# Performance work log

Measured on AMD Instinct MI355X. Metric: run time of the kernel, lower is better.

## Reference

```python
import jax, jax.numpy as jnp
import numpy as np

B, E, N, D, L = 16, 1024, 2048, 256, 3


def setup_inputs() -> dict:
    key = jax.random.key(0)
    ks = jax.random.split(key, 8)
    return {
        "evidences_mat": jax.random.normal(ks[0], (B, E, D), jnp.float32),
        "entities_mat": jax.random.normal(ks[1], (B, N, D), jnp.float32),
        "ev_to_ent": jax.random.bernoulli(ks[2], 0.05, (B, E, N)).astype(jnp.float32),
        "ent_to_ev": jax.random.bernoulli(ks[3], 0.05, (B, N, E)).astype(jnp.float32),
        "w_weight": jax.random.normal(ks[4], (L, D, D), jnp.float32) * 0.05,
        "w_bias": jax.random.normal(ks[5], (L, D), jnp.float32) * 0.05,
        "watt_weight": jax.random.normal(ks[6], (L, D, D), jnp.float32) * 0.05,
        "watt_bias": jax.random.normal(ks[7], (L, D), jnp.float32) * 0.05,
    }


def reference(evidences_mat, entities_mat, ev_to_ent, ent_to_ev,
              w_weight, w_bias, watt_weight, watt_bias):
    ev, ent = evidences_mat, entities_mat
    for i in range(L):
        # attention projections (torch Linear: x @ W.T + b)
        pe = jnp.einsum('bed,od->beo', ev, watt_weight[i]) + watt_bias[i]   # [B,E,D]
        pn = jnp.einsum('bnd,od->bno', ent, watt_weight[i]) + watt_bias[i]  # [B,N,D]
        # evidences -> entities messages
        ev_att = jnp.einsum('bed,bnd->ben', pe, pn) * ev_to_ent             # [B,E,N]
        ev_att = jax.nn.softmax(ev_att, axis=1)                              # over E (dim=1)
        msg_ent = jnp.einsum('ben,bed->bnd', ev_att, ev)                     # [B,N,D]
        msg_ent = jnp.einsum('bnd,od->bno', msg_ent, w_weight[i]) + w_bias[i]
        self_ent = jnp.einsum('bnd,od->bno', ent, w_weight[i]) + w_bias[i]
        ent = jax.nn.relu(msg_ent + self_ent)
        # entities -> evidences messages (uses UPDATED entities, as in source)
        ent_att = jnp.einsum('bnd,bed->bne', pn, pe) * ent_to_ev            # [B,N,E]
        ent_att = jax.nn.softmax(ent_att, axis=1)                            # over N (dim=1)
        msg_ev = jnp.einsum('bne,bnd->bed', ent_att, ent)                    # [B,E,D]
        msg_ev = jnp.einsum('bed,od->beo', msg_ev, w_weight[i]) + w_bias[i]
        self_ev = jnp.einsum('bed,od->beo', ev, w_weight[i]) + w_bias[i]
        ev = jax.nn.relu(msg_ev + self_ev)
        # dropout is a no-op (p=0.0 / eval)
    return ent, ev
```

## Files before the change

kernel.cpp:

```cpp
#include <hip/hip_runtime.h>

#define BB 16
#define EE 1024
#define NN 2048
#define DD 256
#define LL 3
#define NW (NN / 32)

typedef _Float16 half8 __attribute__((ext_vector_type(8)));
typedef _Float16 half4 __attribute__((ext_vector_type(4)));
typedef _Float16 half2_t __attribute__((ext_vector_type(2)));
typedef float f32x4 __attribute__((ext_vector_type(4)));

__device__ __forceinline__ void pmerge(float& m, float& s, float m2, float s2) {
    float nm = fmaxf(m, m2);
    s = s * __expf(m - nm) + s2 * __expf(m2 - nm);
    m = nm;
}

__device__ __forceinline__ unsigned pk2(_Float16 a, _Float16 b) {
    union { _Float16 h[2]; unsigned u; } x;
    x.h[0] = a; x.h[1] = b;
    return x.u;
}

__global__ void split_cast(const float* __restrict__ in, _Float16* __restrict__ hi,
                           _Float16* __restrict__ lo, size_t n) {
    size_t stride = (size_t)gridDim.x * blockDim.x * 4;
    for (size_t i = ((size_t)blockIdx.x * blockDim.x + threadIdx.x) * 4; i < n; i += stride) {
        float4 v = *(const float4*)&in[i];
        half4 hh, ll;
        _Float16 h;
        h = (_Float16)v.x; hh[0] = h; ll[0] = (_Float16)(v.x - (float)h);
        h = (_Float16)v.y; hh[1] = h; ll[1] = (_Float16)(v.y - (float)h);
        h = (_Float16)v.z; hh[2] = h; ll[2] = (_Float16)(v.z - (float)h);
        h = (_Float16)v.w; hh[3] = h; ll[3] = (_Float16)(v.w - (float)h);
        *(half4*)&hi[i] = hh;
        *(half4*)&lo[i] = ll;
    }
}

__global__ void pack_f32(const float* __restrict__ in, unsigned* __restrict__ out, size_t n) {
    size_t stride = (size_t)gridDim.x * blockDim.x;
    int lane = threadIdx.x & 63;
    for (size_t i = (size_t)blockIdx.x * blockDim.x + threadIdx.x; i < n; i += stride) {
        unsigned long long b = __ballot(in[i] != 0.f);
        if (lane == 0) out[i >> 5] = (unsigned)b;
        else if (lane == 32) out[i >> 5] = (unsigned)(b >> 32);
    }
}
__global__ void pack_u8(const unsigned char* __restrict__ in, unsigned* __restrict__ out, size_t n) {
    size_t stride = (size_t)gridDim.x * blockDim.x;
    int lane = threadIdx.x & 63;
    for (size_t i = (size_t)blockIdx.x * blockDim.x + threadIdx.x; i < n; i += stride) {
        unsigned long long b = __ballot(in[i] != 0);
        if (lane == 0) out[i >> 5] = (unsigned)b;
        else if (lane == 32) out[i >> 5] = (unsigned)(b >> 32);
    }
}

__global__ void transpose_split(const float* __restrict__ in, _Float16* __restrict__ oh,
                                _Float16* __restrict__ olo, int R, int C) {
    int b = blockIdx.z;
    int c0 = blockIdx.x * 64, r0 = blockIdx.y * 64;
    const float* ib = in + (size_t)b * R * C;
    size_t ob = (size_t)b * R * C;
    __shared__ float tile[64][65];
    int t = threadIdx.x;
    int cl = t & 63, rb = t >> 6;
#pragma unroll
    for (int j = 0; j < 16; j++) {
        int rl = rb + j * 4;
        tile[rl][cl] = ib[(size_t)(r0 + rl) * C + c0 + cl];
    }
    __syncthreads();
    int oc = t >> 2, q = t & 3;
    half8 h0, h1, l0, l1;
#pragma unroll
    for (int i = 0; i < 8; i++) {
        float v = tile[q * 16 + i][oc];
        _Float16 h = (_Float16)v;
        h0[i] = h; l0[i] = (_Float16)(v - (float)h);
    }
#pragma unroll
    for (int i = 0; i < 8; i++) {
        float v = tile[q * 16 + 8 + i][oc];
        _Float16 h = (_Float16)v;
        h1[i] = h; l1[i] = (_Float16)(v - (float)h);
    }
    size_t o = ob + (size_t)(c0 + oc) * R + r0 + q * 16;
    *(half8*)&oh[o] = h0; *(half8*)&oh[o + 8] = h1;
    *(half8*)&olo[o] = l0; *(half8*)&olo[o + 8] = l1;
}

__global__ void transpose_split_perm(const float* __restrict__ in, _Float16* __restrict__ oh,
                                     _Float16* __restrict__ olo, int R, int C) {
    int b = blockIdx.z;
    int c0 = blockIdx.x * 64, r0 = blockIdx.y * 64;
    const float* ib = in + (size_t)b * R * C;
    size_t ob = (size_t)b * R * C;
    __shared__ float tile[64][65];
    int t = threadIdx.x;
    int cl = t & 63, rb = t >> 6;
#pragma unroll
    for (int j = 0; j < 16; j++) {
        int rl = rb + j * 4;
        tile[rl][cl] = ib[(size_t)(r0 + rl) * C + c0 + cl];
    }
    __syncthreads();
    int oc = t >> 2, q = t & 3;
    int g = q >> 1, sub = q & 1;
#pragma unroll
    for (int j = 0; j < 8; j++) {
        int x = sub * 8 + j;
        float v1 = tile[g * 32 + x][oc];
        float v2 = tile[g * 32 + x + 16][oc];
        _Float16 a = (_Float16)v1, b2 = (_Float16)v2;
        _Float16 la = (_Float16)(v1 - (float)a), lb = (_Float16)(v2 - (float)b2);
        size_t o = ob + (size_t)(c0 + oc) * R + r0 + g * 32 + 2 * x;
        half2_t hp; hp[0] = a; hp[1] = b2;
        half2_t lp; lp[0] = la; lp[1] = lb;
        *(half2_t*)&oh[o] = hp;
        *(half2_t*)&olo[o] = lp;
    }
}

__global__ void transpose_u8(const float* __restrict__ in, unsigned char* __restrict__ out,
                             int R, int C) {
    int b = blockIdx.z;
    int c0 = blockIdx.x * 64, r0 = blockIdx.y * 64;
    const float* ib = in + (size_t)b * R * C;
    unsigned char* ob = out + (size_t)b * R * C;
    __shared__ float tile[64][65];
    int t = threadIdx.x;
    int cl = t & 63, rb = t >> 6;
#pragma unroll
    for (int j = 0; j < 16; j++) {
        int rl = rb + j * 4;
        tile[rl][cl] = ib[(size_t)(r0 + rl) * C + c0 + cl];
    }
    __syncthreads();
    int oc = t >> 2, q = t & 3;
    union { unsigned char b[16]; uint4 v; } u;
#pragma unroll
    for (int i = 0; i < 16; i++) u.b[i] = (unsigned char)tile[q * 16 + i][oc];
    size_t o = (size_t)(c0 + oc) * R + r0 + q * 16;
    *(uint4*)&ob[o] = u.v;
}

template <bool A_SPLIT, bool B_SPLIT, bool HAS_BIAS, bool RELU, bool HAS_ADD,
          bool WRITE_F32, bool WRITE_SPLIT, bool B_BATCHED>
__global__ __launch_bounds__(256) void gemm_nt(
    const _Float16* __restrict__ Ah, const _Float16* __restrict__ Al,
    const _Float16* __restrict__ Bh, const _Float16* __restrict__ Bl,
    const float* __restrict__ bias, float bscale,
    const float* __restrict__ addsrc,
    float* __restrict__ Cf, _Float16* __restrict__ Chi, _Float16* __restrict__ Clo,
    int M, int Nn, int K) {
    const int bz = blockIdx.z;
    const int m0 = blockIdx.x * 128, n0 = blockIdx.y * 128;
    const int t = threadIdx.x, lane = t & 63, wid = t >> 6;
    const int wm = wid >> 1, wn = wid & 1;
    const size_t offA = (size_t)bz * M * K;
    const size_t offB = B_BATCHED ? (size_t)bz * Nn * K : (size_t)0;
    const _Float16* Abh = Ah + offA;
    const _Float16* Abl = A_SPLIT ? (Al + offA) : nullptr;
    const _Float16* Bbh = Bh + offB;
    const _Float16* Bbl = B_SPLIT ? (Bl + offB) : nullptr;

    __shared__ _Float16 sAh[128 * 32];
    __shared__ _Float16 sBh[128 * 32];
    __shared__ _Float16 sAl[A_SPLIT ? 128 * 32 : 1];
    __shared__ _Float16 sBl[B_SPLIT ? 128 * 32 : 1];

    f32x4 acc[4][4] = {};
    const int nk = K >> 5;

    auto gA = [&](const _Float16* base, int kt, int q) {
        return *(const uint4*)(base + (size_t)(m0 + (q >> 2)) * K + (kt << 5) + ((q & 3) << 3));
    };
    auto gB = [&](const _Float16* base, int kt, int q) {
        return *(const uint4*)(base + (size_t)(n0 + (q >> 2)) * K + (kt << 5) + ((q & 3) << 3));
    };

    uint4 rah0 = gA(Abh, 0, t), rah1 = gA(Abh, 0, t + 256);
    uint4 rbh0 = gB(Bbh, 0, t), rbh1 = gB(Bbh, 0, t + 256);
    uint4 ral0 = {}, ral1 = {}, rbl0 = {}, rbl1 = {};
    if (A_SPLIT) { ral0 = gA(Abl, 0, t); ral1 = gA(Abl, 0, t + 256); }
    if (B_SPLIT) { rbl0 = gB(Bbl, 0, t); rbl1 = gB(Bbl, 0, t + 256); }

    for (int kt = 0; kt < nk; ++kt) {
        __syncthreads();
        ((uint4*)sAh)[t] = rah0; ((uint4*)sAh)[t + 256] = rah1;
        ((uint4*)sBh)[t] = rbh0; ((uint4*)sBh)[t + 256] = rbh1;
        if (A_SPLIT) { ((uint4*)sAl)[t] = ral0; ((uint4*)sAl)[t + 256] = ral1; }
        if (B_SPLIT) { ((uint4*)sBl)[t] = rbl0; ((uint4*)sBl)[t + 256] = rbl1; }
        __syncthreads();
        if (kt + 1 < nk) {
            rah0 = gA(Abh, kt + 1, t); rah1 = gA(Abh, kt + 1, t + 256);
            rbh0 = gB(Bbh, kt + 1, t); rbh1 = gB(Bbh, kt + 1, t + 256);
            if (A_SPLIT) { ral0 = gA(Abl, kt + 1, t); ral1 = gA(Abl, kt + 1, t + 256); }
            if (B_SPLIT) { rbl0 = gB(Bbl, kt + 1, t); rbl1 = gB(Bbl, kt + 1, t + 256); }
        }
        half8 afh[4], bfh[4], afl[4], bfl[4];
#pragma unroll
        for (int mi = 0; mi < 4; mi++) {
            int off = (wm * 64 + mi * 16 + (lane & 15)) * 32 + ((lane >> 4) << 3);
            afh[mi] = *(const half8*)&sAh[off];
            if (A_SPLIT) afl[mi] = *(const half8*)&sAl[off];
        }
#pragma unroll
        for (int nj = 0; nj < 4; nj++) {
            int off = (wn * 64 + nj * 16 + (lane & 15)) * 32 + ((lane >> 4) << 3);
            bfh[nj] = *(const half8*)&sBh[off];
            if (B_SPLIT) bfl[nj] = *(const half8*)&sBl[off];
        }
#pragma unroll
        for (int mi = 0; mi < 4; mi++)
#pragma unroll
            for (int nj = 0; nj < 4; nj++) {
                acc[mi][nj] = __builtin_amdgcn_mfma_f32_16x16x32_f16(afh[mi], bfh[nj], acc[mi][nj], 0, 0, 0);
                if (B_SPLIT)
                    acc[mi][nj] = __builtin_amdgcn_mfma_f32_16x16x32_f16(afh[mi], bfl[nj], acc[mi][nj], 0, 0, 0);
                if (A_SPLIT)
                    acc[mi][nj] = __builtin_amdgcn_mfma_f32_16x16x32_f16(afl[mi], bfh[nj], acc[mi][nj], 0, 0, 0);
            }
    }

    const int rbase = (lane >> 4) * 4, cc = lane & 15;
#pragma unroll
    for (int mi = 0; mi < 4; mi++) {
#pragma unroll
        for (int nj = 0; nj < 4; nj++) {
            int gn = n0 + wn * 64 + nj * 16 + cc;
            float bv = HAS_BIAS ? bias[gn] * bscale : 0.f;
#pragma unroll
            for (int r = 0; r < 4; r++) {
                int gm = m0 + wm * 64 + mi * 16 + rbase + r;
                float v = acc[mi][nj][r];
                if (HAS_BIAS) v += bv;
                size_t off = ((size_t)bz * M + gm) * Nn + gn;
                if (HAS_ADD) v += addsrc[off];
                if (RELU) v = fmaxf(v, 0.f);
                if (WRITE_F32) Cf[off] = v;
                if (WRITE_SPLIT) {
                    _Float16 h = (_Float16)v;
                    Chi[off] = h;
                    Clo[off] = (_Float16)(v - (float)h);
                }
            }
        }
    }
}

template <bool TRANSA>
__global__ __launch_bounds__(256) void fused_agg(
    const float* __restrict__ S_, const unsigned* __restrict__ Mk,
    const float2* __restrict__ st, const _Float16* __restrict__ Bh,
    const _Float16* __restrict__ Bl, const float* __restrict__ addsrc,
    _Float16* __restrict__ Xhi, _Float16* __restrict__ Xlo,
    int M, int K) {
    const int bz = blockIdx.z;
    const int m0 = blockIdx.x * 64, n0 = blockIdx.y * 128;
    const int t = threadIdx.x, lane = t & 63, wid = t >> 6;
    const int wm = wid >> 1, wn = wid & 1;
    const float* Sb = S_ + (size_t)bz * EE * NN;
    const unsigned* Mb = Mk + (size_t)bz * EE * NW;
    const float2* stb = st + (size_t)bz * M;
    const _Float16* Bbh = Bh + (size_t)bz * DD * K;
    const _Float16* Bbl = Bl + (size_t)bz * DD * K;

    __shared__ _Float16 sA[64 * 32];
    __shared__ _Float16 sBh[128 * 32];
    __shared__ _Float16 sBl[128 * 32];

    f32x4 acc[2][4] = {};
    const int nk = K >> 5;

    float stc[4], stem[4];
    if (TRANSA) {
        int ncol = (t & 15) * 4;
#pragma unroll
        for (int i = 0; i < 4; i++) {
            float2 v = stb[m0 + ncol + i];
            stc[i] = v.x; stem[i] = v.y;
        }
    } else {
#pragma unroll
        for (int p = 0; p < 2; p++) {
            float2 v = stb[m0 + (t >> 3) + p * 32];
            stc[p] = v.x; stem[p] = v.y;
        }
    }

    struct RawA { f32x4 s1, s2; unsigned a1, a2; };
    RawA A0, A1;
    uint4 rbh0, rbh1, rbl0, rbl1;

    auto prefA_load = [&](RawA& R, int kt) {
        if (TRANSA) {
            int r = t >> 4, ncol = (t & 15) * 4;
            size_t rowoff = (size_t)(kt * 32 + r) * NN + m0 + ncol;
            R.s1 = *(const f32x4*)(Sb + rowoff);
            R.s2 = *(const f32x4*)(Sb + rowoff + (size_t)16 * NN);
            size_t mrow = (size_t)(kt * 32 + r) * NW + (m0 >> 5) + (ncol >> 5);
            R.a1 = Mb[mrow];
            R.a2 = Mb[mrow + (size_t)16 * NW];
        } else {
            int kc = (t & 7) * 4, rb = t >> 3;
            size_t ro1 = (size_t)(m0 + rb) * NN + kt * 32 + kc;
            size_t ro2 = (size_t)(m0 + rb + 32) * NN + kt * 32 + kc;
            R.s1 = *(const f32x4*)(Sb + ro1);
            R.s2 = *(const f32x4*)(Sb + ro2);
            size_t mw1 = (size_t)(m0 + rb) * NW + kt;
            R.a1 = Mb[mw1];
            R.a2 = Mb[mw1 + (size_t)32 * NW];
        }
    };
    auto prefB = [&](int kt) {
        auto g = [&](const _Float16* base, int q) {
            return *(const uint4*)(base + (size_t)(n0 + (q >> 2)) * K + kt * 32 + (q & 3) * 8);
        };
        rbh0 = g(Bbh, t); rbh1 = g(Bbh, t + 256);
        rbl0 = g(Bbl, t); rbl1 = g(Bbl, t + 256);
    };
    auto storeA = [&](RawA& R) {
        if (TRANSA) {
            int r = t >> 4, ncol = (t & 15) * 4;
            unsigned nib1 = (R.a1 >> (ncol & 31)) & 0xFu;
            unsigned nib2 = (R.a2 >> (ncol & 31)) & 0xFu;
#pragma unroll
            for (int i = 0; i < 4; i++) {
                float c = stc[i], em = stem[i];
                float x1 = ((nib1 >> i) & 1u) ? __expf(R.s1[i] - c) : em;
                float x2 = ((nib2 >> i) & 1u) ? __expf(R.s2[i] - c) : em;
                int n = ncol + i;
                int cp = (r >> 2) ^ ((n >> 2) & 3);
                ((unsigned*)sA)[n * 16 + cp * 4 + (r & 3)] = pk2((_Float16)x1, (_Float16)x2);
            }
        } else {
            int kc = (t & 7) * 4, rb = t >> 3;
            unsigned nib1 = (R.a1 >> kc) & 0xFu;
            unsigned nib2 = (R.a2 >> kc) & 0xFu;
            {
                float c = stc[0], em = stem[0];
                _Float16 h0 = (_Float16)((nib1 & 1u) ? __expf(R.s1[0] - c) : em);
                _Float16 h1 = (_Float16)(((nib1 >> 1) & 1u) ? __expf(R.s1[1] - c) : em);
                _Float16 h2 = (_Float16)(((nib1 >> 2) & 1u) ? __expf(R.s1[2] - c) : em);
                _Float16 h3 = (_Float16)(((nib1 >> 3) & 1u) ? __expf(R.s1[3] - c) : em);
                unsigned* dst = (unsigned*)&sA[rb * 32 + kc];
                dst[0] = pk2(h0, h1); dst[1] = pk2(h2, h3);
            }
            {
                float c = stc[1], em = stem[1];
                _Float16 h0 = (_Float16)((nib2 & 1u) ? __expf(R.s2[0] - c) : em);
                _Float16 h1 = (_Float16)(((nib2 >> 1) & 1u) ? __expf(R.s2[1] - c) : em);
                _Float16 h2 = (_Float16)(((nib2 >> 2) & 1u) ? __expf(R.s2[2] - c) : em);
                _Float16 h3 = (_Float16)(((nib2 >> 3) & 1u) ? __expf(R.s2[3] - c) : em);
                unsigned* dst = (unsigned*)&sA[(rb + 32) * 32 + kc];
                dst[0] = pk2(h0, h1); dst[1] = pk2(h2, h3);
            }
        }
    };
    auto storeB = [&]() {
        ((uint4*)sBh)[t] = rbh0; ((uint4*)sBh)[t + 256] = rbh1;
        ((uint4*)sBl)[t] = rbl0; ((uint4*)sBl)[t + 256] = rbl1;
    };
    auto compute = [&]() {
        half8 af[2], bfh[4], bfl[4];
        const int l4 = lane & 15, h = lane >> 4;
        const int cswz = TRANSA ? (h ^ ((l4 >> 2) & 3)) : h;
#pragma unroll
        for (int mi = 0; mi < 2; mi++)
            af[mi] = *(const half8*)&sA[(wm * 32 + mi * 16 + l4) * 32 + cswz * 8];
#pragma unroll
        for (int nj = 0; nj < 4; nj++) {
            int off = (wn * 64 + nj * 16 + l4) * 32 + h * 8;
            bfh[nj] = *(const half8*)&sBh[off];
            bfl[nj] = *(const half8*)&sBl[off];
        }
#pragma unroll
        for (int mi = 0; mi < 2; mi++)
#pragma unroll
            for (int nj = 0; nj < 4; nj++) {
                acc[mi][nj] = __builtin_amdgcn_mfma_f32_16x16x32_f16(af[mi], bfh[nj], acc[mi][nj], 0, 0, 0);
                acc[mi][nj] = __builtin_amdgcn_mfma_f32_16x16x32_f16(af[mi], bfl[nj], acc[mi][nj], 0, 0, 0);
            }
    };

    prefA_load(A0, 0);
    prefA_load(A1, 1);
    prefB(0);

    for (int kt = 0; kt < nk; kt += 2) {
        __syncthreads();
        storeA(A0); storeB();
        __syncthreads();
        if (kt + 2 < nk) prefA_load(A0, kt + 2);
        prefB(kt + 1);
        compute();
        __syncthreads();
        storeA(A1); storeB();
        __syncthreads();
        if (kt + 3 < nk) prefA_load(A1, kt + 3);
        if (kt + 2 < nk) prefB(kt + 2);
        compute();
    }

    const int rbase = (lane >> 4) * 4, cc = lane & 15;
#pragma unroll
    for (int mi = 0; mi < 2; mi++) {
#pragma unroll
        for (int nj = 0; nj < 4; nj++) {
            int gn = n0 + wn * 64 + nj * 16 + cc;
#pragma unroll
            for (int r = 0; r < 4; r++) {
                int gm = m0 + wm * 32 + mi * 16 + rbase + r;
                size_t off = ((size_t)bz * M + gm) * DD + gn;
                float v = acc[mi][nj][r] + addsrc[off];
                _Float16 h = (_Float16)v;
                Xhi[off] = h;
                Xlo[off] = (_Float16)(v - (float)h);
            }
        }
    }
}

__global__ __launch_bounds__(256) void stats(const float* __restrict__ S_,
                                             const unsigned* __restrict__ mb1,
                                             const unsigned* __restrict__ mb2,
                                             float2* __restrict__ d1p,
                                             float2* __restrict__ d2p) {
    int b = blockIdx.z, e0 = blockIdx.y * 64, n0 = blockIdx.x * 256;
    int t = threadIdx.x, lane = t & 63, w = t >> 6;
    size_t base = ((size_t)b * EE + e0) * NN + n0;
    const unsigned* M1 = mb1 + (size_t)b * EE * NW;
    const unsigned* M2 = mb2 + (size_t)b * EE * NW;
    const int wordb = (n0 >> 5) + (lane >> 3);
    const int sh = (lane & 7) * 4;

    f32x4 xs[16];
    unsigned int am[16], cm[16];
#pragma unroll
    for (int j = 0; j < 16; j++) {
        size_t off = base + (size_t)(w * 16 + j) * NN + lane * 4;
        float4 s = *(const float4*)(S_ + off);
        xs[j][0] = s.x; xs[j][1] = s.y; xs[j][2] = s.z; xs[j][3] = s.w;
        size_t mrow = (size_t)(e0 + w * 16 + j) * NW + wordb;
        am[j] = (M1[mrow] >> sh) & 0xFu;
        cm[j] = (M2[mrow] >> sh) & 0xFu;
    }

    float cmx[4], csm[4];
#pragma unroll
    for (int i = 0; i < 4; i++) {
        float mx = ((am[0] >> i) & 1u) ? xs[0][i] : 0.f;
#pragma unroll
        for (int j = 1; j < 16; j++) {
            float xe = ((am[j] >> i) & 1u) ? xs[j][i] : 0.f;
            mx = fmaxf(mx, xe);
        }
        float sm = 0.f;
#pragma unroll
        for (int j = 0; j < 16; j++) {
            float xe = ((am[j] >> i) & 1u) ? xs[j][i] : 0.f;
            sm += __expf(xe - mx);
        }
        cmx[i] = mx; csm[i] = sm;
    }
    __shared__ float rm[4][256], rs[4][256];
#pragma unroll
    for (int i = 0; i < 4; i++) { rm[w][lane * 4 + i] = cmx[i]; rs[w][lane * 4 + i] = csm[i]; }
    __syncthreads();
    {
        float M0 = rm[0][t], S0 = rs[0][t];
#pragma unroll
        for (int ww = 1; ww < 4; ww++) pmerge(M0, S0, rm[ww][t], rs[ww][t]);
        d1p[(size_t)blockIdx.y * (BB * NN) + (size_t)b * NN + n0 + t] = make_float2(M0, S0);
    }

#pragma unroll
    for (int j = 0; j < 16; j++) {
        float x0 = (cm[j] & 1u) ? xs[j][0] : 0.f;
        float x1 = ((cm[j] >> 1) & 1u) ? xs[j][1] : 0.f;
        float x2 = ((cm[j] >> 2) & 1u) ? xs[j][2] : 0.f;
        float x3 = ((cm[j] >> 3) & 1u) ? xs[j][3] : 0.f;
        float mx = fmaxf(fmaxf(x0, x1), fmaxf(x2, x3));
#pragma unroll
        for (int off = 1; off < 64; off <<= 1) mx = fmaxf(mx, __shfl_xor(mx, off, 64));
        float sm = __expf(x0 - mx) + __expf(x1 - mx) + __expf(x2 - mx) + __expf(x3 - mx);
#pragma unroll
        for (int off = 1; off < 64; off <<= 1) sm += __shfl_xor(sm, off, 64);
        if (lane == 0)
            d2p[(size_t)blockIdx.x * (BB * EE) + (size_t)b * EE + e0 + w * 16 + j] = make_float2(mx, sm);
    }
}

__global__ void reduce_dens(const float2* __restrict__ d1p, const float2* __restrict__ d2p,
                            float2* __restrict__ d1, float2* __restrict__ d2) {
    int i = blockIdx.x * 256 + threadIdx.x;
    if (i < BB * NN) {
        float2 v = d1p[i];
        float m = v.x, s = v.y;
#pragma unroll
        for (int k = 1; k < 16; k++) {
            float2 u = d1p[(size_t)k * (BB * NN) + i];
            pmerge(m, s, u.x, u.y);
        }
        float c = m + __logf(s);
        d1[i] = make_float2(c, __expf(-c));
    } else {
        int j = i - BB * NN;
        if (j < BB * EE) {
            float2 v = d2p[j];
            float m = v.x, s = v.y;
#pragma unroll
            for (int k = 1; k < 8; k++) {
                float2 u = d2p[(size_t)k * (BB * EE) + j];
                pmerge(m, s, u.x, u.y);
            }
            float c = m + __logf(s);
            d2[j] = make_float2(c, __expf(-c));
        }
    }
}

extern "C" void kernel_launch(void* const* d_in, const int* in_sizes, int n_in,
                              void* d_out, int out_size, void* d_ws, size_t ws_size,
                              hipStream_t stream) {
    const float* evid   = (const float*)d_in[0];
    const float* enti   = (const float*)d_in[1];
    const float* ev2ent = (const float*)d_in[2];
    const float* ent2ev = (const float*)d_in[3];
    const float* w_w    = (const float*)d_in[4];
    const float* w_b    = (const float*)d_in[5];
    const float* wa_w   = (const float*)d_in[6];
    const float* wa_b   = (const float*)d_in[7];
    float* out_ent = (float*)d_out;
    float* out_ev  = out_ent + (size_t)BB * NN * DD;

    char* p = (char*)d_ws;
    auto alloc = [&](size_t bytes) {
        char* r = p;
        p += (bytes + 255) & ~(size_t)255;
        return (void*)r;
    };
    const size_t nED = (size_t)BB * EE * DD, nND = (size_t)BB * NN * DD;
    const size_t nEN = (size_t)BB * EE * NN, nW = (size_t)LL * DD * DD;
    _Float16* Whi  = (_Float16*)alloc(nW * 2);
    _Float16* Wlo  = (_Float16*)alloc(nW * 2);
    _Float16* Wahi = (_Float16*)alloc(nW * 2);
    _Float16* Walo = (_Float16*)alloc(nW * 2);
    _Float16* evh  = (_Float16*)alloc(nED * 2);
    _Float16* evl  = (_Float16*)alloc(nED * 2);
    _Float16* enth = (_Float16*)alloc(nND * 2);
    _Float16* entl = (_Float16*)alloc(nND * 2);
    _Float16* evTh = (_Float16*)alloc(nED * 2);
    _Float16* evTl = (_Float16*)alloc(nED * 2);
    _Float16* entTh= (_Float16*)alloc(nND * 2);
    _Float16* entTl= (_Float16*)alloc(nND * 2);
    _Float16* peh  = (_Float16*)alloc(nED * 2);
    _Float16* pel  = (_Float16*)alloc(nED * 2);
    _Float16* pnh  = (_Float16*)alloc(nND * 2);
    _Float16* pnl  = (_Float16*)alloc(nND * 2);
    float*    S    = (float*)alloc(nEN * 4);
    unsigned char* m2t_u8 = (unsigned char*)alloc(nEN);
    unsigned* mb1 = (unsigned*)alloc(nEN / 8);
    unsigned* mb2 = (unsigned*)alloc(nEN / 8);
    float* evS  = (float*)alloc(nED * 4);
    float* entS = (float*)alloc(nND * 4);
    float2* d1p = (float2*)alloc((size_t)16 * BB * NN * 8);
    float2* d2p = (float2*)alloc((size_t)8 * BB * EE * 8);
    float2* d1  = (float2*)alloc((size_t)BB * NN * 8);
    float2* d2  = (float2*)alloc((size_t)BB * EE * 8);
    if ((size_t)(p - (char*)d_ws) > ws_size) return;
    _Float16* Xenth = pnh; _Float16* Xentl = pnl;
    _Float16* Xevh  = peh; _Float16* Xevl  = pel;

    split_cast<<<2048, 256, 0, stream>>>(wa_w, Wahi, Walo, nW);
    split_cast<<<2048, 256, 0, stream>>>(w_w, Whi, Wlo, nW);
    split_cast<<<2048, 256, 0, stream>>>(evid, evh, evl, nED);
    split_cast<<<2048, 256, 0, stream>>>(enti, enth, entl, nND);
    pack_f32<<<2048, 256, 0, stream>>>(ev2ent, mb1, nEN);
    transpose_u8<<<dim3(EE / 64, NN / 64, BB), 256, 0, stream>>>(ent2ev, m2t_u8, NN, EE);
    pack_u8<<<2048, 256, 0, stream>>>(m2t_u8, mb2, nEN);
    transpose_split_perm<<<dim3(DD / 64, EE / 64, BB), 256, 0, stream>>>(evid, evTh, evTl, EE, DD);
    hipMemcpyAsync(evS, evid, nED * 4, hipMemcpyDeviceToDevice, stream);
    hipMemcpyAsync(entS, enti, nND * 4, hipMemcpyDeviceToDevice, stream);

    for (int i = 0; i < LL; i++) {
        const _Float16* Wih  = Whi + (size_t)i * DD * DD;
        const _Float16* Wil  = Wlo + (size_t)i * DD * DD;
        const _Float16* Waih = Wahi + (size_t)i * DD * DD;
        const _Float16* Wail = Walo + (size_t)i * DD * DD;
        const float* bi  = w_b + i * DD;
        const float* bai = wa_b + i * DD;

        gemm_nt<true, true, true, false, false, false, true, false>
            <<<dim3(EE / 128, DD / 128, BB), 256, 0, stream>>>(
                evh, evl, Waih, Wail, bai, 1.f, nullptr, nullptr, peh, pel, EE, DD, DD);
        gemm_nt<true, true, true, false, false, false, true, false>
            <<<dim3(NN / 128, DD / 128, BB), 256, 0, stream>>>(
                enth, entl, Waih, Wail, bai, 1.f, nullptr, nullptr, pnh, pnl, NN, DD, DD);
        gemm_nt<true, true, false, false, false, true, false, true>
            <<<dim3(EE / 128, NN / 128, BB), 256, 0, stream>>>(
                peh, pel, pnh, pnl, nullptr, 0.f, nullptr, S, nullptr, nullptr, EE, NN, DD);
        stats<<<dim3(NN / 256, EE / 64, BB), 256, 0, stream>>>(S, mb1, mb2, d1p, d2p);
        reduce_dens<<<(BB * NN + BB * EE + 255) / 256, 256, 0, stream>>>(d1p, d2p, d1, d2);
        fused_agg<true><<<dim3(NN / 64, 2, BB), 256, 0, stream>>>(
            S, mb1, d1, evTh, evTl, entS, Xenth, Xentl, NN, EE);
        float* entDst = (i == LL - 1) ? out_ent : entS;
        gemm_nt<true, true, true, true, false, true, true, false>
            <<<dim3(NN / 128, DD / 128, BB), 256, 0, stream>>>(
                Xenth, Xentl, Wih, Wil, bi, 2.f, nullptr, entDst, enth, entl, NN, DD, DD);
        transpose_split<<<dim3(DD / 64, NN / 64, BB), 256, 0, stream>>>(entDst, entTh, entTl, NN, DD);
        fused_agg<false><<<dim3(EE / 64, 2, BB), 256, 0, stream>>>(
            S, mb2, d2, entTh, entTl, evS, Xevh, Xevl, EE, NN);
        float* evDst = (i == LL - 1) ? out_ev : evS;
        gemm_nt<true, true, true, true, false, true, true, false>
            <<<dim3(EE / 128, DD / 128, BB), 256, 0, stream>>>(
                Xevh, Xevl, Wih, Wil, bi, 2.f, nullptr, evDst, evh, evl, EE, DD, DD);
        if (i < LL - 1)
            transpose_split_perm<<<dim3(DD / 64, EE / 64, BB), 256, 0, stream>>>(evS, evTh, evTl, EE, DD);
    }
}
```

Baseline: 1.372 ms.

## Widen fused_agg N-tile to full D so the softmax A tile is built once

fused_agg previously split the D=256 output dimension across two blocks, so each block re-read the fp32 score matrix and mask and recomputed exp for the same A tile. Each block now covers all 256 output columns: the transposed variant keeps a 64-row M tile with 8 N fragments per wave, and the non-transposed variant shrinks to a 32-row M tile with each of the four waves owning 64 columns. This halves reads of S and the mask and halves the exp work. In exchange it doubles the B tile in shared memory, raises accumulator register pressure (possibly lowering occupancy), and halves the number of blocks in the grid.

```diff
diff --git a/kernel.cpp b/kernel.cpp
--- a/kernel.cpp
+++ b/kernel.cpp
@@ -260,21 +260,24 @@
     const _Float16* __restrict__ Bl, const float* __restrict__ addsrc,
     _Float16* __restrict__ Xhi, _Float16* __restrict__ Xlo,
     int M, int K) {
+    constexpr int MT = TRANSA ? 64 : 32;
+    constexpr int NJ = TRANSA ? 8 : 4;
     const int bz = blockIdx.z;
-    const int m0 = blockIdx.x * 64, n0 = blockIdx.y * 128;
+    const int m0 = blockIdx.x * MT;
     const int t = threadIdx.x, lane = t & 63, wid = t >> 6;
-    const int wm = wid >> 1, wn = wid & 1;
+    const int wm = TRANSA ? (wid >> 1) : 0;
+    const int wnoff = TRANSA ? ((wid & 1) * 128) : (wid * 64);
     const float* Sb = S_ + (size_t)bz * EE * NN;
     const unsigned* Mb = Mk + (size_t)bz * EE * NW;
     const float2* stb = st + (size_t)bz * M;
     const _Float16* Bbh = Bh + (size_t)bz * DD * K;
     const _Float16* Bbl = Bl + (size_t)bz * DD * K;
 
-    __shared__ _Float16 sA[64 * 32];
-    __shared__ _Float16 sBh[128 * 32];
-    __shared__ _Float16 sBl[128 * 32];
-
-    f32x4 acc[2][4] = {};
+    __shared__ _Float16 sA[MT * 32];
+    __shared__ _Float16 sBh[256 * 32];
+    __shared__ _Float16 sBl[256 * 32];
+
+    f32x4 acc[2][NJ] = {};
     const int nk = K >> 5;
 
     float stc[4], stem[4];
@@ -286,16 +289,13 @@
             stc[i] = v.x; stem[i] = v.y;
         }
     } else {
-#pragma unroll
-        for (int p = 0; p < 2; p++) {
-            float2 v = stb[m0 + (t >> 3) + p * 32];
-            stc[p] = v.x; stem[p] = v.y;
-        }
+        float2 v = stb[m0 + (t >> 3)];
+        stc[0] = v.x; stem[0] = v.y;
     }
 
     struct RawA { f32x4 s1, s2; unsigned a1, a2; };
     RawA A0, A1;
-    uint4 rbh0, rbh1, rbl0, rbl1;
+    uint4 rbh[4], rbl[4];
 
     auto prefA_load = [&](RawA& R, int kt) {
         if (TRANSA) {
@@ -308,21 +308,19 @@
             R.a2 = Mb[mrow + (size_t)16 * NW];
         } else {
             int kc = (t & 7) * 4, rb = t >> 3;
-            size_t ro1 = (size_t)(m0 + rb) * NN + kt * 32 + kc;
-            size_t ro2 = (size_t)(m0 + rb + 32) * NN + kt * 32 + kc;
-            R.s1 = *(const f32x4*)(Sb + ro1);
-            R.s2 = *(const f32x4*)(Sb + ro2);
-            size_t mw1 = (size_t)(m0 + rb) * NW + kt;
-            R.a1 = Mb[mw1];
-            R.a2 = Mb[mw1 + (size_t)32 * NW];
+            size_t ro = (size_t)(m0 + rb) * NN + kt * 32 + kc;
+            R.s1 = *(const f32x4*)(Sb + ro);
+            R.a1 = Mb[(size_t)(m0 + rb) * NW + kt];
         }
     };
     auto prefB = [&](int kt) {
-        auto g = [&](const _Float16* base, int q) {
-            return *(const uint4*)(base + (size_t)(n0 + (q >> 2)) * K + kt * 32 + (q & 3) * 8);
-        };
-        rbh0 = g(Bbh, t); rbh1 = g(Bbh, t + 256);
-        rbl0 = g(Bbl, t); rbl1 = g(Bbl, t + 256);
+#pragma unroll
+        for (int c = 0; c < 4; c++) {
+            int q = t + 256 * c;
+            size_t o = (size_t)(q >> 2) * K + kt * 32 + (q & 3) * 8;
+            rbh[c] = *(const uint4*)(Bbh + o);
+            rbl[c] = *(const uint4*)(Bbl + o);
+        }
     };
     auto storeA = [&](RawA& R) {
         if (TRANSA) {
@@ -340,49 +338,40 @@
             }
         } else {
             int kc = (t & 7) * 4, rb = t >> 3;
-            unsigned nib1 = (R.a1 >> kc) & 0xFu;
-            unsigned nib2 = (R.a2 >> kc) & 0xFu;
-            {
-                float c = stc[0], em = stem[0];
-                _Float16 h0 = (_Float16)((nib1 & 1u) ? __expf(R.s1[0] - c) : em);
-                _Float16 h1 = (_Float16)(((nib1 >> 1) & 1u) ? __expf(R.s1[1] - c) : em);
-                _Float16 h2 = (_Float16)(((nib1 >> 2) & 1u) ? __expf(R.s1[2] - c) : em);
-                _Float16 h3 = (_Float16)(((nib1 >> 3) & 1u) ? __expf(R.s1[3] - c) : em);
-                unsigned* dst = (unsigned*)&sA[rb * 32 + kc];
-                dst[0] = pk2(h0, h1); dst[1] = pk2(h2, h3);
-            }
-            {
-                float c = stc[1], em = stem[1];
-                _Float16 h0 = (_Float16)((nib2 & 1u) ? __expf(R.s2[0] - c) : em);
-                _Float16 h1 = (_Float16)(((nib2 >> 1) & 1u) ? __expf(R.s2[1] - c) : em);
-                _Float16 h2 = (_Float16)(((nib2 >> 2) & 1u) ? __expf(R.s2[2] - c) : em);
-                _Float16 h3 = (_Float16)(((nib2 >> 3) & 1u) ? __expf(R.s2[3] - c) : em);
-                unsigned* dst = (unsigned*)&sA[(rb + 32) * 32 + kc];
-                dst[0] = pk2(h0, h1); dst[1] = pk2(h2, h3);
-            }
+            unsigned nib = (R.a1 >> kc) & 0xFu;
+            float c = stc[0], em = stem[0];
+            _Float16 h0 = (_Float16)((nib & 1u) ? __expf(R.s1[0] - c) : em);
+            _Float16 h1 = (_Float16)(((nib >> 1) & 1u) ? __expf(R.s1[1] - c) : em);
+            _Float16 h2 = (_Float16)(((nib >> 2) & 1u) ? __expf(R.s1[2] - c) : em);
+            _Float16 h3 = (_Float16)(((nib >> 3) & 1u) ? __expf(R.s1[3] - c) : em);
+            unsigned* dst = (unsigned*)&sA[rb * 32 + kc];
+            dst[0] = pk2(h0, h1); dst[1] = pk2(h2, h3);
         }
     };
     auto storeB = [&]() {
-        ((uint4*)sBh)[t] = rbh0; ((uint4*)sBh)[t + 256] = rbh1;
-        ((uint4*)sBl)[t] = rbl0; ((uint4*)sBl)[t + 256] = rbl1;
+#pragma unroll
+        for (int c = 0; c < 4; c++) {
+            ((uint4*)sBh)[t + 256 * c] = rbh[c];
+            ((uint4*)sBl)[t + 256 * c] = rbl[c];
+        }
     };
     auto compute = [&]() {
-        half8 af[2], bfh[4], bfl[4];
+        half8 af[2], bfh[NJ], bfl[NJ];
         const int l4 = lane & 15, h = lane >> 4;
         const int cswz = TRANSA ? (h ^ ((l4 >> 2) & 3)) : h;
 #pragma unroll
         for (int mi = 0; mi < 2; mi++)
             af[mi] = *(const half8*)&sA[(wm * 32 + mi * 16 + l4) * 32 + cswz * 8];
 #pragma unroll
-        for (int nj = 0; nj < 4; nj++) {
-            int off = (wn * 64 + nj * 16 + l4) * 32 + h * 8;
+        for (int nj = 0; nj < NJ; nj++) {
+            int off = (wnoff + nj * 16 + l4) * 32 + h * 8;
             bfh[nj] = *(const half8*)&sBh[off];
             bfl[nj] = *(const half8*)&sBl[off];
         }
 #pragma unroll
         for (int mi = 0; mi < 2; mi++)
 #pragma unroll
-            for (int nj = 0; nj < 4; nj++) {
+            for (int nj = 0; nj < NJ; nj++) {
                 acc[mi][nj] = __builtin_amdgcn_mfma_f32_16x16x32_f16(af[mi], bfh[nj], acc[mi][nj], 0, 0, 0);
                 acc[mi][nj] = __builtin_amdgcn_mfma_f32_16x16x32_f16(af[mi], bfl[nj], acc[mi][nj], 0, 0, 0);
             }
@@ -411,8 +400,8 @@
 #pragma unroll
     for (int mi = 0; mi < 2; mi++) {
 #pragma unroll
-        for (int nj = 0; nj < 4; nj++) {
-            int gn = n0 + wn * 64 + nj * 16 + cc;
+        for (int nj = 0; nj < NJ; nj++) {
+            int gn = wnoff + nj * 16 + cc;
 #pragma unroll
             for (int r = 0; r < 4; r++) {
                 int gm = m0 + wm * 32 + mi * 16 + rbase + r;
@@ -607,14 +596,14 @@
                 peh, pel, pnh, pnl, nullptr, 0.f, nullptr, S, nullptr, nullptr, EE, NN, DD);
         stats<<<dim3(NN / 256, EE / 64, BB), 256, 0, stream>>>(S, mb1, mb2, d1p, d2p);
         reduce_dens<<<(BB * NN + BB * EE + 255) / 256, 256, 0, stream>>>(d1p, d2p, d1, d2);
-        fused_agg<true><<<dim3(NN / 64, 2, BB), 256, 0, stream>>>(
+        fused_agg<true><<<dim3(NN / 64, 1, BB), 256, 0, stream>>>(
             S, mb1, d1, evTh, evTl, entS, Xenth, Xentl, NN, EE);
         float* entDst = (i == LL - 1) ? out_ent : entS;
         gemm_nt<true, true, true, true, false, true, true, false>
             <<<dim3(NN / 128, DD / 128, BB), 256, 0, stream>>>(
                 Xenth, Xentl, Wih, Wil, bi, 2.f, nullptr, entDst, enth, entl, NN, DD, DD);
         transpose_split<<<dim3(DD / 64, NN / 64, BB), 256, 0, stream>>>(entDst, entTh, entTl, NN, DD);
-        fused_agg<false><<<dim3(EE / 64, 2, BB), 256, 0, stream>>>(
+        fused_agg<false><<<dim3(EE / 32, 1, BB), 256, 0, stream>>>(
             S, mb2, d2, entTh, entTl, evS, Xevh, Xevl, EE, NN);
         float* evDst = (i == LL - 1) ? out_ev : evS;
         gemm_nt<true, true, true, true, false, true, true, false>
```

Result: slower. 2.883 ms (+110.1%).
